# Performance work log

Measured on AMD Instinct MI355X. Metric: run time of the kernel, lower is better.

## Reference

```python
import jax, jax.numpy as jnp
import numpy as np

B, H, L, D = 2, 16, 2048, 64


def setup_inputs() -> dict:
    key = jax.random.key(0)
    kq, kk, kv = jax.random.split(key, 3)
    return {
        "query": jax.random.normal(kq, (B, H, L, D), dtype=jnp.float32),
        "key": jax.random.normal(kk, (B, H, L, D), dtype=jnp.float32),
        "value": jax.random.normal(kv, (B, H, L, D), dtype=jnp.float32),
        "dhead": D,
        "causal": 1,
    }


def reference(query, key, value, dhead, causal):
    # mode='dhead': muP attention with scale 1/dhead (not 1/sqrt(dhead)).
    # Inputs/outputs in [B, H, L, D] layout (the torch code transposes to
    # [B, L, H, D] for the einsum and transposes back; net layout is the same).
    scale = 1.0 / dhead
    a = jnp.einsum('bhld,bhLd->bhlL', query, key) * scale  # [B,H,L,L]
    if causal:
        seq = a.shape[-1]
        mask = jnp.tril(jnp.ones((seq, seq), dtype=bool))  # [L,L]
        a = jnp.where(mask, a, jnp.float32(-jnp.inf))
    a = jax.nn.softmax(a, axis=-1)
    out = jnp.einsum('bhlL,bhLd->bhld', a, value)  # [B,H,L,D]
    return out
```

## Files before the change

kernel.cpp:

```cpp
#include <hip/hip_runtime.h>

#define BHH 32
#define SEQ 2048
#define DH 64
#define BQ 64
#define BK 64
#define NKT (SEQ / BK)
#define NQB (SEQ / BQ)
#define NT  (BHH * NKT)

typedef __attribute__((ext_vector_type(8))) _Float16 half8_t;
typedef __attribute__((ext_vector_type(4))) _Float16 half4_t;
typedef __attribute__((ext_vector_type(4))) float f32x4;

__device__ __forceinline__ void async_copy16(const void* g, const void* lds) {
    __builtin_amdgcn_global_load_lds(
        (const __attribute__((address_space(1))) unsigned int*)g,
        (__attribute__((address_space(3))) unsigned int*)lds, 16, 0, 0);
}

__global__ __launch_bounds__(256) void prep_kv(const float* __restrict__ K,
                                               const float* __restrict__ V,
                                               _Float16* __restrict__ Kf,
                                               _Float16* __restrict__ Vf) {
    __shared__ _Float16 l[64 * 76];
    const int t = threadIdx.x;
    const int wave = t >> 6, lane = t & 63, ln15 = lane & 15, quad = lane >> 4;
    const int row = t >> 2, col0 = (t & 3) * 16;
    int b = blockIdx.x;

    if (b < NT) {
        const float4* src = (const float4*)(K + (size_t)b * 4096 + row * 64 + col0);
        #pragma unroll
        for (int q = 0; q < 2; ++q) {
            float4 f0 = src[q * 2], f1 = src[q * 2 + 1];
            half8_t w = { (_Float16)f0.x, (_Float16)f0.y, (_Float16)f0.z, (_Float16)f0.w,
                          (_Float16)f1.x, (_Float16)f1.y, (_Float16)f1.z, (_Float16)f1.w };
            *(half8_t*)&l[row * 72 + col0 + q * 8] = w;
        }
        __syncthreads();
        #pragma unroll
        for (int p = 0; p < 2; ++p) {
            const int bid = wave * 2 + p, c = bid >> 1, k0 = bid & 1;
            half8_t w = *(const half8_t*)&l[(c * 16 + ln15) * 72 + k0 * 32 + quad * 8];
            *(half8_t*)&Kf[(size_t)b * 4096 + bid * 512 + lane * 8] = w;
        }
    } else {
        b -= NT;
        const float4* src = (const float4*)(V + (size_t)b * 4096 + row * 64 + col0);
        #pragma unroll
        for (int q = 0; q < 4; ++q) {
            float4 f = src[q];
            half4_t w = { (_Float16)f.x, (_Float16)f.y, (_Float16)f.z, (_Float16)f.w };
            *(half4_t*)&l[row * 76 + col0 + q * 4] = w;
        }
        __syncthreads();
        #pragma unroll
        for (int p = 0; p < 4; ++p) {
            const int f = wave * 4 + p, cn = f >> 2, c = f & 3;
            half4_t w;
            #pragma unroll
            for (int j = 0; j < 4; ++j)
                w[j] = l[(c * 16 + quad * 4 + j) * 76 + cn * 16 + ln15];
            *(half4_t*)&Vf[(size_t)b * 4096 + f * 256 + lane * 4] = w;
        }
    }
}

__global__ __launch_bounds__(256) void fattn_kernel(
        const float* __restrict__ Q, const _Float16* __restrict__ Kf,
        const _Float16* __restrict__ Vf, float* __restrict__ O) {
    const int bh = blockIdx.x & 31;
    const int r = blockIdx.x >> 5, j = r & 7, rnd = r >> 3;
    const int qb = (rnd == 0) ? 31 - j : (rnd == 1) ? 16 + j
                 : (rnd == 2) ? 15 - j : j;
    const int tid  = threadIdx.x;
    const int wave = tid >> 6;
    const int lane = tid & 63;
    const int ln15 = lane & 15;
    const int quad = lane >> 4;

    __shared__ _Float16 ldsK[2][4096];
    __shared__ _Float16 ldsV[2][4096];

    const size_t base = (size_t)bh * SEQ * DH;
    const int q0   = qb * BQ;
    const int qrow = q0 + wave * 16;

    const float qscale = 1.44269504f / 64.0f;
    half8_t qfrag[2];
    {
        const float* qp = Q + base + (size_t)(qrow + ln15) * DH + quad * 8;
        #pragma unroll
        for (int k0 = 0; k0 < 2; ++k0) {
            float4 a = *(const float4*)(qp + k0 * 32);
            float4 b = *(const float4*)(qp + k0 * 32 + 4);
            qfrag[k0] = (half8_t){
                (_Float16)(a.x * qscale), (_Float16)(a.y * qscale),
                (_Float16)(a.z * qscale), (_Float16)(a.w * qscale),
                (_Float16)(b.x * qscale), (_Float16)(b.y * qscale),
                (_Float16)(b.z * qscale), (_Float16)(b.w * qscale) };
        }
    }

    f32x4 acc[4] = {};
    float l_i = 0.f;
    const size_t tb = (size_t)(bh * NKT) * 4096;

    #define STAGE(kt_, b_) do {                                              \
        const size_t toff = tb + (size_t)(kt_) * 4096;                       \
        _Pragma("unroll")                                                    \
        for (int i_ = 0; i_ < 4; ++i_) {                                     \
            const int bid_ = wave * 4 + i_;                                  \
            if (bid_ < 8)                                                    \
                async_copy16(Kf + toff + bid_ * 512 + lane * 8,              \
                             &ldsK[b_][bid_ * 512]);                         \
            else                                                             \
                async_copy16(Vf + toff + (bid_ - 8) * 512 + lane * 8,        \
                             &ldsV[b_][(bid_ - 8) * 512]);                   \
        }                                                                    \
    } while (0)

    const int nkt = qb + 1;
    STAGE(0, 0);
    __syncthreads();

    for (int kt = 0; kt < nkt; ++kt) {
        const _Float16* kvk = ldsK[kt & 1];
        const _Float16* kvv = ldsV[kt & 1];
        if (kt + 1 < nkt) STAGE(kt + 1, (kt + 1) & 1);

        f32x4 st[4];
        #pragma unroll
        for (int c = 0; c < 4; ++c) {
            half8_t kf0 = *(const half8_t*)&kvk[(c * 2 + 0) * 512 + lane * 8];
            half8_t kf1 = *(const half8_t*)&kvk[(c * 2 + 1) * 512 + lane * 8];
            f32x4 a = {};
            a = __builtin_amdgcn_mfma_f32_16x16x32_f16(kf0, qfrag[0], a, 0, 0, 0);
            a = __builtin_amdgcn_mfma_f32_16x16x32_f16(kf1, qfrag[1], a, 0, 0, 0);
            st[c] = a;
        }

        const int kbase = kt * BK;
        const bool needmask = (kt == qb);
        const int rowi = qrow + ln15;
        half4_t pfrag[4];
        float psum = 0.f;
        #pragma unroll
        for (int c = 0; c < 4; ++c) {
            #pragma unroll
            for (int rr = 0; rr < 4; ++rr) {
                float v = __builtin_amdgcn_exp2f(st[c][rr]);
                if (needmask && (kbase + c * 16 + quad * 4 + rr) > rowi) v = 0.f;
                pfrag[c][rr] = (_Float16)v;
                psum += v;
            }
        }
        psum += __shfl_xor(psum, 16);
        psum += __shfl_xor(psum, 32);
        l_i += psum;

        #pragma unroll
        for (int cn = 0; cn < 4; ++cn) {
            #pragma unroll
            for (int c = 0; c < 4; ++c) {
                half4_t vf = *(const half4_t*)&kvv[(cn * 4 + c) * 256 + lane * 4];
                acc[cn] = __builtin_amdgcn_mfma_f32_16x16x16f16(vf, pfrag[c], acc[cn], 0, 0, 0);
            }
        }
        __syncthreads();
    }

    {
        const float rl = 1.0f / l_i;
        float* op = O + base + (size_t)(qrow + ln15) * DH;
        #pragma unroll
        for (int cn = 0; cn < 4; ++cn) {
            float4 o;
            o.x = acc[cn][0] * rl;
            o.y = acc[cn][1] * rl;
            o.z = acc[cn][2] * rl;
            o.w = acc[cn][3] * rl;
            *(float4*)(op + cn * 16 + quad * 4) = o;
        }
    }
    #undef STAGE
}

extern "C" void kernel_launch(void* const* d_in, const int* in_sizes, int n_in,
                              void* d_out, int out_size, void* d_ws, size_t ws_size,
                              hipStream_t stream) {
    const float* Q = (const float*)d_in[0];
    const float* K = (const float*)d_in[1];
    const float* V = (const float*)d_in[2];
    float* O = (float*)d_out;
    _Float16* Kf = (_Float16*)d_ws;
    _Float16* Vf = Kf + (size_t)NT * 4096;
    prep_kv<<<2 * NT, 256, 0, stream>>>(K, V, Kf, Vf);
    fattn_kernel<<<NQB * BHH, 256, 0, stream>>>(Q, Kf, Vf, O);
}
```

Baseline: 129.7 us.

## Use 128-row query tiles with 8 waves splitting keys and LDS reduction

Doubles the query tile to 128 rows and the block to 512 threads. Each wave owns 32 query rows and half of each 64-key tile, and the two key halves are merged through shared memory at the end. Each K/V tile staged in LDS is now reused by twice as many query rows, which cuts global and LDS traffic per output. In exchange the grid has half as many blocks, adds a final cross-wave reduction, and leaves some waves idle on diagonal tiles.

```diff
diff --git a/kernel.cpp b/kernel.cpp
--- a/kernel.cpp
+++ b/kernel.cpp
@@ -3,7 +3,7 @@
 #define BHH 32
 #define SEQ 2048
 #define DH 64
-#define BQ 64
+#define BQ 128
 #define BK 64
 #define NKT (SEQ / BK)
 #define NQB (SEQ / BQ)
@@ -67,35 +67,37 @@
     }
 }
 
-__global__ __launch_bounds__(256) void fattn_kernel(
+__global__ __launch_bounds__(512) void fattn_kernel(
         const float* __restrict__ Q, const _Float16* __restrict__ Kf,
         const _Float16* __restrict__ Vf, float* __restrict__ O) {
     const int bh = blockIdx.x & 31;
-    const int r = blockIdx.x >> 5, j = r & 7, rnd = r >> 3;
-    const int qb = (rnd == 0) ? 31 - j : (rnd == 1) ? 16 + j
-                 : (rnd == 2) ? 15 - j : j;
+    const int r  = blockIdx.x >> 5;
+    const int qb = (r < 8) ? (15 - r) : (r - 8);
     const int tid  = threadIdx.x;
     const int wave = tid >> 6;
     const int lane = tid & 63;
     const int ln15 = lane & 15;
     const int quad = lane >> 4;
-
-    __shared__ _Float16 ldsK[2][4096];
-    __shared__ _Float16 ldsV[2][4096];
+    const int sq = wave & 3;
+    const int sk = wave >> 2;
+
+    __shared__ __align__(16) float smemF[8832 + 128];
+    _Float16* ldsH = (_Float16*)smemF;
 
     const size_t base = (size_t)bh * SEQ * DH;
-    const int q0   = qb * BQ;
-    const int qrow = q0 + wave * 16;
+    const int q0 = qb * BQ;
+    const int qw = q0 + sq * 32;
 
     const float qscale = 1.44269504f / 64.0f;
-    half8_t qfrag[2];
-    {
-        const float* qp = Q + base + (size_t)(qrow + ln15) * DH + quad * 8;
+    half8_t qfrag[2][2];
+    #pragma unroll
+    for (int g = 0; g < 2; ++g) {
+        const float* qp = Q + base + (size_t)(qw + g * 16 + ln15) * DH + quad * 8;
         #pragma unroll
         for (int k0 = 0; k0 < 2; ++k0) {
             float4 a = *(const float4*)(qp + k0 * 32);
             float4 b = *(const float4*)(qp + k0 * 32 + 4);
-            qfrag[k0] = (half8_t){
+            qfrag[g][k0] = (half8_t){
                 (_Float16)(a.x * qscale), (_Float16)(a.y * qscale),
                 (_Float16)(a.z * qscale), (_Float16)(a.w * qscale),
                 (_Float16)(b.x * qscale), (_Float16)(b.y * qscale),
@@ -103,85 +105,115 @@
         }
     }
 
-    f32x4 acc[4] = {};
-    float l_i = 0.f;
+    f32x4 acc[2][4] = {};
+    float l_i[2] = {0.f, 0.f};
     const size_t tb = (size_t)(bh * NKT) * 4096;
 
     #define STAGE(kt_, b_) do {                                              \
         const size_t toff = tb + (size_t)(kt_) * 4096;                       \
         _Pragma("unroll")                                                    \
-        for (int i_ = 0; i_ < 4; ++i_) {                                     \
-            const int bid_ = wave * 4 + i_;                                  \
+        for (int i_ = 0; i_ < 2; ++i_) {                                     \
+            const int bid_ = wave * 2 + i_;                                  \
             if (bid_ < 8)                                                    \
                 async_copy16(Kf + toff + bid_ * 512 + lane * 8,              \
-                             &ldsK[b_][bid_ * 512]);                         \
+                             &ldsH[(b_) * 8192 + bid_ * 512]);               \
             else                                                             \
                 async_copy16(Vf + toff + (bid_ - 8) * 512 + lane * 8,        \
-                             &ldsV[b_][(bid_ - 8) * 512]);                   \
+                             &ldsH[(b_) * 8192 + 4096 + (bid_ - 8) * 512]);  \
         }                                                                    \
     } while (0)
 
-    const int nkt = qb + 1;
+    const int nkt = 2 * qb + 2;
     STAGE(0, 0);
     __syncthreads();
 
     for (int kt = 0; kt < nkt; ++kt) {
-        const _Float16* kvk = ldsK[kt & 1];
-        const _Float16* kvv = ldsV[kt & 1];
+        const _Float16* kvk = &ldsH[(kt & 1) * 8192];
+        const _Float16* kvv = kvk + 4096;
         if (kt + 1 < nkt) STAGE(kt + 1, (kt + 1) & 1);
 
-        f32x4 st[4];
-        #pragma unroll
-        for (int c = 0; c < 4; ++c) {
-            half8_t kf0 = *(const half8_t*)&kvk[(c * 2 + 0) * 512 + lane * 8];
-            half8_t kf1 = *(const half8_t*)&kvk[(c * 2 + 1) * 512 + lane * 8];
-            f32x4 a = {};
-            a = __builtin_amdgcn_mfma_f32_16x16x32_f16(kf0, qfrag[0], a, 0, 0, 0);
-            a = __builtin_amdgcn_mfma_f32_16x16x32_f16(kf1, qfrag[1], a, 0, 0, 0);
-            st[c] = a;
-        }
-
-        const int kbase = kt * BK;
-        const bool needmask = (kt == qb);
-        const int rowi = qrow + ln15;
-        half4_t pfrag[4];
-        float psum = 0.f;
-        #pragma unroll
-        for (int c = 0; c < 4; ++c) {
-            #pragma unroll
-            for (int rr = 0; rr < 4; ++rr) {
-                float v = __builtin_amdgcn_exp2f(st[c][rr]);
-                if (needmask && (kbase + c * 16 + quad * 4 + rr) > rowi) v = 0.f;
-                pfrag[c][rr] = (_Float16)v;
-                psum += v;
-            }
-        }
-        psum += __shfl_xor(psum, 16);
-        psum += __shfl_xor(psum, 32);
-        l_i += psum;
-
-        #pragma unroll
-        for (int cn = 0; cn < 4; ++cn) {
-            #pragma unroll
-            for (int c = 0; c < 4; ++c) {
-                half4_t vf = *(const half4_t*)&kvv[(cn * 4 + c) * 256 + lane * 4];
-                acc[cn] = __builtin_amdgcn_mfma_f32_16x16x16f16(vf, pfrag[c], acc[cn], 0, 0, 0);
+        const int kw = kt * 64 + sk * 32;
+        if (kw <= qw + 31) {
+            f32x4 st[2][2];
+            #pragma unroll
+            for (int c = 0; c < 2; ++c) {
+                const int cg = sk * 2 + c;
+                half8_t kf0 = *(const half8_t*)&kvk[(cg * 2 + 0) * 512 + lane * 8];
+                half8_t kf1 = *(const half8_t*)&kvk[(cg * 2 + 1) * 512 + lane * 8];
+                #pragma unroll
+                for (int g = 0; g < 2; ++g) {
+                    f32x4 a = {};
+                    a = __builtin_amdgcn_mfma_f32_16x16x32_f16(kf0, qfrag[g][0], a, 0, 0, 0);
+                    a = __builtin_amdgcn_mfma_f32_16x16x32_f16(kf1, qfrag[g][1], a, 0, 0, 0);
+                    st[c][g] = a;
+                }
+            }
+
+            const bool needmask = (kw + 31) > qw;
+            half4_t pfrag[2][2];
+            #pragma unroll
+            for (int g = 0; g < 2; ++g) {
+                const int rowi = qw + g * 16 + ln15;
+                float psum = 0.f;
+                #pragma unroll
+                for (int c = 0; c < 2; ++c) {
+                    #pragma unroll
+                    for (int rr = 0; rr < 4; ++rr) {
+                        float v = __builtin_amdgcn_exp2f(st[c][g][rr]);
+                        if (needmask && (kw + c * 16 + quad * 4 + rr) > rowi) v = 0.f;
+                        pfrag[c][g][rr] = (_Float16)v;
+                        psum += v;
+                    }
+                }
+                psum += __shfl_xor(psum, 16);
+                psum += __shfl_xor(psum, 32);
+                l_i[g] += psum;
+            }
+
+            #pragma unroll
+            for (int cn = 0; cn < 4; ++cn) {
+                #pragma unroll
+                for (int c = 0; c < 2; ++c) {
+                    const int f = cn * 4 + sk * 2 + c;
+                    half4_t vf = *(const half4_t*)&kvv[f * 256 + lane * 4];
+                    acc[0][cn] = __builtin_amdgcn_mfma_f32_16x16x16f16(vf, pfrag[c][0], acc[0][cn], 0, 0, 0);
+                    acc[1][cn] = __builtin_amdgcn_mfma_f32_16x16x16f16(vf, pfrag[c][1], acc[1][cn], 0, 0, 0);
+                }
             }
         }
         __syncthreads();
     }
 
-    {
-        const float rl = 1.0f / l_i;
-        float* op = O + base + (size_t)(qrow + ln15) * DH;
-        #pragma unroll
-        for (int cn = 0; cn < 4; ++cn) {
-            float4 o;
-            o.x = acc[cn][0] * rl;
-            o.y = acc[cn][1] * rl;
-            o.z = acc[cn][2] * rl;
-            o.w = acc[cn][3] * rl;
-            *(float4*)(op + cn * 16 + quad * 4) = o;
+    if (sk == 1) {
+        #pragma unroll
+        for (int g = 0; g < 2; ++g) {
+            const int row = sq * 32 + g * 16 + ln15;
+            #pragma unroll
+            for (int cn = 0; cn < 4; ++cn) {
+                float* p = &smemF[row * 68 + cn * 16 + quad * 4];
+                p[0] = acc[g][cn][0]; p[1] = acc[g][cn][1];
+                p[2] = acc[g][cn][2]; p[3] = acc[g][cn][3];
+            }
+            smemF[8832 + row] = l_i[g];
+        }
+    }
+    __syncthreads();
+    if (sk == 0) {
+        #pragma unroll
+        for (int g = 0; g < 2; ++g) {
+            const int row = sq * 32 + g * 16 + ln15;
+            const float rl = 1.0f / (l_i[g] + smemF[8832 + row]);
+            float* op = O + base + (size_t)(qw + g * 16 + ln15) * DH;
+            #pragma unroll
+            for (int cn = 0; cn < 4; ++cn) {
+                const float* p = &smemF[row * 68 + cn * 16 + quad * 4];
+                float4 o;
+                o.x = (acc[g][cn][0] + p[0]) * rl;
+                o.y = (acc[g][cn][1] + p[1]) * rl;
+                o.z = (acc[g][cn][2] + p[2]) * rl;
+                o.w = (acc[g][cn][3] + p[3]) * rl;
+                *(float4*)(op + cn * 16 + quad * 4) = o;
+            }
         }
     }
     #undef STAGE
@@ -197,5 +229,5 @@
     _Float16* Kf = (_Float16*)d_ws;
     _Float16* Vf = Kf + (size_t)NT * 4096;
     prep_kv<<<2 * NT, 256, 0, stream>>>(K, V, Kf, Vf);
-    fattn_kernel<<<NQB * BHH, 256, 0, stream>>>(Q, Kf, Vf, O);
-}
+    fattn_kernel<<<NQB * BHH, 512, 0, stream>>>(Q, Kf, Vf, O);
+}
```

Result: slower. 132.4 us (+2.1%).

## Split long causal query blocks across KV chunks with a combine pass

Applied to the files above, without the earlier changes.

Long query blocks are split into chunks of up to 8 KV tiles, mapped to separate workgroups through a chunk table, which balances work across the causal triangle. Partial outputs (fp16) and row sums are written to workspace, and a new combine kernel sums them and normalises. This removes the long tail of late query blocks. In exchange it adds a third launch, extra global traffic, and fp16 rounding of unnormalised partials. Because there is no max subtraction, the partials can be large and may lose precision or overflow fp16.

```diff
diff --git a/kernel.cpp b/kernel.cpp
--- a/kernel.cpp
+++ b/kernel.cpp
@@ -8,6 +8,9 @@
 #define NKT (SEQ / BK)
 #define NQB (SEQ / BQ)
 #define NT  (BHH * NKT)
+#define TCH 8
+#define NCH 80
+#define NMULTI 72
 
 typedef __attribute__((ext_vector_type(8))) _Float16 half8_t;
 typedef __attribute__((ext_vector_type(4))) _Float16 half4_t;
@@ -17,6 +20,18 @@
     __builtin_amdgcn_global_load_lds(
         (const __attribute__((address_space(1))) unsigned int*)g,
         (__attribute__((address_space(3))) unsigned int*)lds, 16, 0, 0);
+}
+
+__device__ __forceinline__ void chunk_map(int cid, int& qb, int& s) {
+    if (cid < 8)       { qb = 8 + cid;              s = 0; }
+    else if (cid < 24) { qb = 16 + (cid - 8) / 2;   s = (cid - 8) & 1; }
+    else if (cid < 48) { qb = 24 + (cid - 24) / 3;  s = (cid - 24) % 3; }
+    else { const int u = cid - 48; qb = (7 - (u >> 2)) + 8 * (u & 3); s = qb >> 3; }
+}
+__device__ __forceinline__ int pidx_of(int qb, int s) {
+    return (qb < 16) ? (qb - 8) * 2 + s
+         : (qb < 24) ? 16 + (qb - 16) * 3 + s
+         :             40 + (qb - 24) * 4 + s;
 }
 
 __global__ __launch_bounds__(256) void prep_kv(const float* __restrict__ K,
@@ -69,11 +84,16 @@
 
 __global__ __launch_bounds__(256) void fattn_kernel(
         const float* __restrict__ Q, const _Float16* __restrict__ Kf,
-        const _Float16* __restrict__ Vf, float* __restrict__ O) {
-    const int bh = blockIdx.x & 31;
-    const int r = blockIdx.x >> 5, j = r & 7, rnd = r >> 3;
-    const int qb = (rnd == 0) ? 31 - j : (rnd == 1) ? 16 + j
-                 : (rnd == 2) ? 15 - j : j;
+        const _Float16* __restrict__ Vf, float* __restrict__ O,
+        _Float16* __restrict__ Opart, float* __restrict__ Lpart) {
+    const int bh  = blockIdx.x & 31;
+    const int cid = blockIdx.x >> 5;
+    int qb, s;
+    chunk_map(cid, qb, s);
+    const int nc  = (qb >> 3) + 1;
+    const int len = min(TCH, qb + 1 - s * TCH);
+    const int kt0 = s * TCH;
+
     const int tid  = threadIdx.x;
     const int wave = tid >> 6;
     const int lane = tid & 63;
@@ -121,14 +141,14 @@
         }                                                                    \
     } while (0)
 
-    const int nkt = qb + 1;
-    STAGE(0, 0);
+    STAGE(kt0, 0);
     __syncthreads();
 
-    for (int kt = 0; kt < nkt; ++kt) {
-        const _Float16* kvk = ldsK[kt & 1];
-        const _Float16* kvv = ldsV[kt & 1];
-        if (kt + 1 < nkt) STAGE(kt + 1, (kt + 1) & 1);
+    for (int i = 0; i < len; ++i) {
+        const int kt = kt0 + i;
+        const _Float16* kvk = ldsK[i & 1];
+        const _Float16* kvv = ldsV[i & 1];
+        if (i + 1 < len) STAGE(kt + 1, (i + 1) & 1);
 
         f32x4 st[4];
         #pragma unroll
@@ -171,7 +191,7 @@
         __syncthreads();
     }
 
-    {
+    if (nc == 1) {
         const float rl = 1.0f / l_i;
         float* op = O + base + (size_t)(qrow + ln15) * DH;
         #pragma unroll
@@ -183,8 +203,52 @@
             o.w = acc[cn][3] * rl;
             *(float4*)(op + cn * 16 + quad * 4) = o;
         }
+    } else {
+        const int pidx = pidx_of(qb, s);
+        const int row = wave * 16 + ln15;
+        _Float16* pp = Opart + ((size_t)bh * NMULTI + pidx) * 4096 + row * 64;
+        #pragma unroll
+        for (int cn = 0; cn < 4; ++cn) {
+            half4_t h = { (_Float16)acc[cn][0], (_Float16)acc[cn][1],
+                          (_Float16)acc[cn][2], (_Float16)acc[cn][3] };
+            *(half4_t*)(pp + cn * 16 + quad * 4) = h;
+        }
+        if (quad == 0)
+            Lpart[((size_t)bh * NMULTI + pidx) * 64 + row] = l_i;
     }
     #undef STAGE
+}
+
+__global__ __launch_bounds__(256) void combine_kernel(
+        const _Float16* __restrict__ Opart, const float* __restrict__ Lpart,
+        float* __restrict__ O) {
+    const int bh = blockIdx.x & 31;
+    const int qb = 8 + (blockIdx.x >> 5);
+    const int nc = (qb >> 3) + 1;
+    const int pbase = pidx_of(qb, 0);
+    const int t = threadIdx.x;
+    const int row = t >> 2, col0 = (t & 3) * 16;
+
+    const _Float16* P = Opart + ((size_t)bh * NMULTI + pbase) * 4096 + row * 64 + col0;
+    const float* Lp = Lpart + ((size_t)bh * NMULTI + pbase) * 64 + row;
+
+    float acc[16] = {};
+    float l = 0.f;
+    for (int c = 0; c < nc; ++c) {
+        l += Lp[c * 64];
+        half8_t a = *(const half8_t*)(P + c * 4096);
+        half8_t b = *(const half8_t*)(P + c * 4096 + 8);
+        #pragma unroll
+        for (int j = 0; j < 8; ++j) { acc[j] += (float)a[j]; acc[8 + j] += (float)b[j]; }
+    }
+    const float rl = 1.0f / l;
+    float* op = O + ((size_t)bh * SEQ + qb * 64 + row) * DH + col0;
+    #pragma unroll
+    for (int v = 0; v < 4; ++v) {
+        float4 o = { acc[v * 4] * rl, acc[v * 4 + 1] * rl,
+                     acc[v * 4 + 2] * rl, acc[v * 4 + 3] * rl };
+        *(float4*)(op + v * 4) = o;
+    }
 }
 
 extern "C" void kernel_launch(void* const* d_in, const int* in_sizes, int n_in,
@@ -194,8 +258,14 @@
     const float* K = (const float*)d_in[1];
     const float* V = (const float*)d_in[2];
     float* O = (float*)d_out;
-    _Float16* Kf = (_Float16*)d_ws;
-    _Float16* Vf = Kf + (size_t)NT * 4096;
+    char* ws = (char*)d_ws;
+    _Float16* Kf    = (_Float16*)ws;
+    _Float16* Vf    = (_Float16*)(ws + ((size_t)8 << 20));
+    _Float16* Opart = (_Float16*)(ws + ((size_t)16 << 20));
+    float*    Lpart = (float*)(ws + ((size_t)16 << 20)
+                               + (size_t)BHH * NMULTI * 4096 * 2);
+
     prep_kv<<<2 * NT, 256, 0, stream>>>(K, V, Kf, Vf);
-    fattn_kernel<<<NQB * BHH, 256, 0, stream>>>(Q, Kf, Vf, O);
-}
+    fattn_kernel<<<NCH * BHH, 256, 0, stream>>>(Q, Kf, Vf, O, Opart, Lpart);
+    combine_kernel<<<24 * BHH, 256, 0, stream>>>(Opart, Lpart, O);
+}
```

Result: slower. 136.2 us (+5.0%).
